# Performance work log

Hardware: AMD Instinct MI355X
Metric: run time of the kernel (lower is better)

The kernel has to match this reference:

```python
import jax, jax.numpy as jnp
import numpy as np

LN_EPS = 1e-12


def _layernorm(x, gamma, beta):
    mu = jnp.mean(x, axis=-1, keepdims=True)
    var = jnp.var(x, axis=-1, keepdims=True)
    return gamma * (x - mu) / jnp.sqrt(var + LN_EPS) + beta


def setup_inputs() -> dict:
    key = jax.random.key(0)
    ks = jax.random.split(key, 8)
    B, N, C, H = 8, 8192, 512, 8
    FFN = 4 * C
    s_attn = 1.0 / np.sqrt(C)
    s_ffn1 = 1.0 / np.sqrt(C)
    s_ffn2 = 1.0 / np.sqrt(FFN)
    return {
        "x": jax.random.normal(ks[0], (B, N, C), jnp.float32),
        "wq": jax.random.normal(ks[1], (C, C), jnp.float32) * s_attn,
        "bq": jnp.zeros((C,), jnp.float32),
        "wk": jax.random.normal(ks[2], (C, C), jnp.float32) * s_attn,
        "bk": jnp.zeros((C,), jnp.float32),
        "wv": jax.random.normal(ks[3], (C, C), jnp.float32) * s_attn,
        "bv": jnp.zeros((C,), jnp.float32),
        "wo": jax.random.normal(ks[4], (C, C), jnp.float32) * s_attn,
        "bo": jnp.zeros((C,), jnp.float32),
        "gamma1": jnp.ones((C,), jnp.float32),
        "beta1": jnp.zeros((C,), jnp.float32),
        "w_fc1": jax.random.normal(ks[5], (C, FFN), jnp.float32) * s_ffn1,
        "b_fc1": jnp.zeros((FFN,), jnp.float32),
        "w_fc2": jax.random.normal(ks[6], (FFN, C), jnp.float32) * s_ffn2,
        "b_fc2": jnp.zeros((C,), jnp.float32),
        "gamma2": jnp.ones((C,), jnp.float32),
        "beta2": jnp.zeros((C,), jnp.float32),
        "window_size": 64,
        "n_head": 8,
    }


def reference(x, wq, bq, wk, bk, wv, bv, wo, bo, gamma1, beta1,
              w_fc1, b_fc1, w_fc2, b_fc2, gamma2, beta2,
              window_size, n_head):
    B, N, C = x.shape
    ws = window_size
    H = n_head
    dh = C // H

    # window partition: [B, N, C] -> [B*N/ws, ws, C]
    xw = x.reshape(B * N // ws, ws, C)
    shortcut = xw

    # windowed multi-head self-attention
    q = (xw @ wq + bq).reshape(-1, ws, H, dh)
    k = (xw @ wk + bk).reshape(-1, ws, H, dh)
    v = (xw @ wv + bv).reshape(-1, ws, H, dh)
    scale = 1.0 / jnp.sqrt(jnp.asarray(dh, xw.dtype))
    attn = jnp.einsum('wqhd,wkhd->whqk', q, k) * scale  # [nw, H, ws, ws]
    attn = jax.nn.softmax(attn, axis=-1)
    out = jnp.einsum('whqk,wkhd->wqhd', attn, v).reshape(-1, ws, C)
    out = out @ wo + bo

    # residual + LN1
    h = _layernorm(out + shortcut, gamma1, beta1)

    # MLP (fc1 -> GELU -> fc2), residual + LN2
    ff = jax.nn.gelu(h @ w_fc1 + b_fc1, approximate=False) @ w_fc2 + b_fc2
    h = _layernorm(ff + h, gamma2, beta2)

    # window reverse: -> [B, N, C]
    return h.reshape(B, N, C)
```

## Files before the change

### kernel.cpp

```cpp
#include <hip/hip_runtime.h>

typedef __attribute__((ext_vector_type(8))) short bf16x8;
typedef __attribute__((ext_vector_type(4))) float f32x4;

__device__ __forceinline__ short f2b(float f) {
  unsigned u = __builtin_bit_cast(unsigned, f);
  unsigned r = (u + 0x7FFFu + ((u >> 16) & 1u)) >> 16;
  return (short)r;
}
__device__ __forceinline__ float b2f(short s) {
  unsigned u = ((unsigned)(unsigned short)s) << 16;
  return __builtin_bit_cast(float, u);
}

__device__ __forceinline__ void gload16(const void* g, void* l) {
  __builtin_amdgcn_global_load_lds(
      (const __attribute__((address_space(1))) void*)g,
      (__attribute__((address_space(3))) void*)l, 16, 0, 0);
}

__device__ __forceinline__ float gelu_f(float v) {
  float u = v * (0.7978845608f + 0.0356774081f * v * v);
  float a = fabsf(u);
  float e = __expf(-2.f * a);
  float t = (1.f - e) * __builtin_amdgcn_rcpf(1.f + e);
  t = (u < 0.f) ? -t : t;
  return 0.5f * v * (1.f + t);
}

__global__ void cvt_bf16_vec(const float* __restrict__ src, short* __restrict__ dst, long n) {
  long i = ((long)blockIdx.x * 256 + threadIdx.x) * 8;
  if (i >= n) return;
  f32x4 a = *(const f32x4*)(src + i);
  f32x4 b = *(const f32x4*)(src + i + 4);
  bf16x8 o;
#pragma unroll
  for (int j = 0; j < 4; j++) o[j] = f2b(a[j]);
#pragma unroll
  for (int j = 0; j < 4; j++) o[j + 4] = f2b(b[j]);
  *(bf16x8*)(dst + i) = o;
}

__global__ void transpose_cvt_t(const float* __restrict__ src, short* __restrict__ dst,
                                int K, int N) {
  __shared__ float tile[32][33];
  const int n0 = blockIdx.x * 32, k0 = blockIdx.y * 32;
  const int j = threadIdx.x & 31, i0 = threadIdx.x >> 5;
#pragma unroll
  for (int r = 0; r < 4; r++) {
    int i = i0 + r * 8;
    tile[i][j] = src[(long)(k0 + i) * N + n0 + j];
  }
  __syncthreads();
#pragma unroll
  for (int r = 0; r < 4; r++) {
    int i = i0 + r * 8;
    dst[(long)(n0 + i) * K + k0 + j] = f2b(tile[j][i]);
  }
}

__global__ void pack_bias3(const float* __restrict__ b0, const float* __restrict__ b1,
                           const float* __restrict__ b2, float* __restrict__ out) {
  int t = blockIdx.x * 256 + threadIdx.x;
  if (t >= 1536) return;
  out[t] = (t < 512) ? b0[t] : ((t < 1024) ? b1[t - 512] : b2[t - 1024]);
}

template <int EPI>
__global__ __launch_bounds__(256, 3) void gemm_bt(
    const short* __restrict__ A, const short* __restrict__ Bt,
    const float* __restrict__ bias, const float* __restrict__ resF,
    const short* __restrict__ resB, void* __restrict__ Cout, int K, int ldc, int gxN) {
  __shared__ short lds[3 * 8192];
  const int t = threadIdx.x;
  const int w = t >> 6, lane = t & 63;
  const int lr = lane & 15, lg = lane >> 4;

  const int nwg = gridDim.x;
  const int orig = blockIdx.x;
  const int q = nwg >> 3, r = nwg & 7, xcd = orig & 7, idx = orig >> 3;
  const int swz = (xcd < r ? xcd * (q + 1) : r * (q + 1) + (xcd - r) * q) + idx;
  const long m0 = (long)(swz / gxN) * 128;
  const int n0 = (swz % gxN) * 128;

  const int wm = (w >> 1) * 64, wn = (w & 1) * 64;

  f32x4 acc[4][4];
#pragma unroll
  for (int i = 0; i < 4; i++)
#pragma unroll
    for (int j = 0; j < 4; j++) acc[i][j] = f32x4{0.f, 0.f, 0.f, 0.f};

  const int srow = t >> 2;
  const int schunk = (t & 3) ^ ((t >> 3) & 3);
  const short* Ag = A + (m0 + srow) * (long)K + schunk * 8;
  const short* Bg = Bt + ((long)n0 + srow) * K + schunk * 8;
  const long half = (long)64 * K;

#define STAGE(b, kt)                                   \
  {                                                    \
    short* d = lds + (b) * 8192 + t * 8;               \
    gload16(Ag + (long)(kt) * 32, d);                  \
    gload16(Ag + half + (long)(kt) * 32, d + 2048);    \
    gload16(Bg + (long)(kt) * 32, d + 4096);           \
    gload16(Bg + half + (long)(kt) * 32, d + 6144);    \
  }

  const int xsw = (lg ^ ((lr >> 1) & 3)) * 8;
  const int aoff = (wm + lr) * 32 + xsw;
  const int boff = 4096 + (wn + lr) * 32 + xsw;

#define TILE_WAIT(WN)                                        \
  asm volatile("s_waitcnt vmcnt(" #WN ")" ::: "memory");     \
  __builtin_amdgcn_sched_barrier(0);                         \
  __builtin_amdgcn_s_barrier();                              \
  __builtin_amdgcn_sched_barrier(0);

#define BODY(CB)                                                               \
  {                                                                            \
    const short* Lb = lds + (CB) * 8192;                                       \
    bf16x8 a[4], b[4];                                                         \
    _Pragma("unroll") for (int mi = 0; mi < 4; mi++)                           \
        a[mi] = *(const bf16x8*)(Lb + aoff + mi * 512);                        \
    _Pragma("unroll") for (int nj = 0; nj < 4; nj++)                           \
        b[nj] = *(const bf16x8*)(Lb + boff + nj * 512);                        \
    __builtin_amdgcn_s_setprio(1);                                             \
    _Pragma("unroll") for (int mi = 0; mi < 4; mi++)                           \
        _Pragma("unroll") for (int nj = 0; nj < 4; nj++) acc[mi][nj] =         \
            __builtin_amdgcn_mfma_f32_16x16x32_bf16(a[mi], b[nj], acc[mi][nj], \
                                                    0, 0, 0);                  \
    __builtin_amdgcn_s_setprio(0);                                             \
  }

  const int NKT = K >> 5;
  STAGE(0, 0)
  STAGE(1, 1)

  int cb = 0, sb = 2;
  for (int kt = 0; kt < NKT - 1; ++kt) {
    TILE_WAIT(4)
    if (kt + 2 < NKT) STAGE(sb, kt + 2)
    BODY(cb)
    cb = (cb == 2) ? 0 : cb + 1;
    sb = (sb == 2) ? 0 : sb + 1;
  }
  TILE_WAIT(0)
  BODY(cb)
#undef STAGE
#undef TILE_WAIT
#undef BODY

  float bv[4];
#pragma unroll
  for (int nj = 0; nj < 4; nj++) bv[nj] = bias[n0 + wn + nj * 16 + lr];

#pragma unroll
  for (int mi = 0; mi < 4; mi++)
#pragma unroll
    for (int i = 0; i < 4; i++) {
      const long row = m0 + wm + mi * 16 + lg * 4 + i;
      const long rb = row * ldc + n0 + wn + lr;
      if (EPI == 0) {
        short* p = (short*)Cout + rb;
#pragma unroll
        for (int nj = 0; nj < 4; nj++) p[nj * 16] = f2b(acc[mi][nj][i] + bv[nj]);
      } else if (EPI == 1) {
        short* p = (short*)Cout + rb;
#pragma unroll
        for (int nj = 0; nj < 4; nj++) p[nj * 16] = f2b(gelu_f(acc[mi][nj][i] + bv[nj]));
      } else if (EPI == 2) {
        float* p = (float*)Cout + rb;
        const float* rp = resF + rb;
#pragma unroll
        for (int nj = 0; nj < 4; nj++) p[nj * 16] = acc[mi][nj][i] + bv[nj] + rp[nj * 16];
      } else {
        float* p = (float*)Cout + rb;
        const short* rp = resB + rb;
#pragma unroll
        for (int nj = 0; nj < 4; nj++)
          p[nj * 16] = acc[mi][nj][i] + bv[nj] + b2f(rp[nj * 16]);
      }
    }
}

__global__ __launch_bounds__(256, 2) void attn_win(const short* __restrict__ QKV,
                                                   short* __restrict__ AO) {
  __shared__ short Vs[64 * 72];
  __shared__ short Ps[64 * 72];
  const int t = threadIdx.x, w = t >> 6, lane = t & 63;
  const int lr = lane & 15, lg = lane >> 4;
  const long base = (long)blockIdx.x * 64 * 1536;
  const long obase = (long)blockIdx.x * 64 * 512;

  for (int h = 0; h < 8; h++) {
    const int co = h * 64;
#pragma unroll
    for (int it = 0; it < 2; it++) {
      int c = t + it * 256;
      int j = c >> 3, d0 = (c & 7) * 8;
      *(bf16x8*)(Vs + j * 72 + d0) =
          *(const bf16x8*)(QKV + base + (long)j * 1536 + 1024 + co + d0);
    }
    __syncthreads();

    bf16x8 qf[2], kf[4][2];
#pragma unroll
    for (int kb = 0; kb < 2; kb++)
      qf[kb] = *(const bf16x8*)(QKV + base + (long)(w * 16 + lr) * 1536 + co + kb * 32 + lg * 8);
#pragma unroll
    for (int nj = 0; nj < 4; nj++)
#pragma unroll
      for (int kb = 0; kb < 2; kb++)
        kf[nj][kb] = *(const bf16x8*)(QKV + base + (long)(nj * 16 + lr) * 1536 + 512 + co +
                                      kb * 32 + lg * 8);

    f32x4 s[4];
#pragma unroll
    for (int nj = 0; nj < 4; nj++) {
      s[nj] = f32x4{0.f, 0.f, 0.f, 0.f};
      s[nj] = __builtin_amdgcn_mfma_f32_16x16x32_bf16(qf[0], kf[nj][0], s[nj], 0, 0, 0);
      s[nj] = __builtin_amdgcn_mfma_f32_16x16x32_bf16(qf[1], kf[nj][1], s[nj], 0, 0, 0);
      s[nj] = s[nj] * 0.125f;
    }

#pragma unroll
    for (int i = 0; i < 4; i++) {
      float mx = fmaxf(fmaxf(s[0][i], s[1][i]), fmaxf(s[2][i], s[3][i]));
#pragma unroll
      for (int off = 1; off < 16; off <<= 1) mx = fmaxf(mx, __shfl_xor(mx, off, 64));
      float sum = 0.f;
#pragma unroll
      for (int nj = 0; nj < 4; nj++) {
        float p = __expf(s[nj][i] - mx);
        s[nj][i] = p;
        sum += p;
      }
#pragma unroll
      for (int off = 1; off < 16; off <<= 1) sum += __shfl_xor(sum, off, 64);
      float inv = 1.f / sum;
#pragma unroll
      for (int nj = 0; nj < 4; nj++) s[nj][i] *= inv;
    }

#pragma unroll
    for (int nj = 0; nj < 4; nj++)
#pragma unroll
      for (int i = 0; i < 4; i++)
        Ps[(w * 16 + lg * 4 + i) * 72 + nj * 16 + lr] = f2b(s[nj][i]);

    bf16x8 pa[2];
#pragma unroll
    for (int kb = 0; kb < 2; kb++)
      pa[kb] = *(const bf16x8*)(Ps + (w * 16 + lr) * 72 + kb * 32 + lg * 8);

    f32x4 o[4];
#pragma unroll
    for (int nb = 0; nb < 4; nb++) o[nb] = f32x4{0.f, 0.f, 0.f, 0.f};
#pragma unroll
    for (int kb = 0; kb < 2; kb++)
#pragma unroll
      for (int nb = 0; nb < 4; nb++) {
        bf16x8 vb;
#pragma unroll
        for (int jj = 0; jj < 8; jj++)
          vb[jj] = Vs[(kb * 32 + lg * 8 + jj) * 72 + nb * 16 + lr];
        o[nb] = __builtin_amdgcn_mfma_f32_16x16x32_bf16(pa[kb], vb, o[nb], 0, 0, 0);
      }

#pragma unroll
    for (int nb = 0; nb < 4; nb++)
#pragma unroll
      for (int i = 0; i < 4; i++)
        AO[obase + (long)(w * 16 + lg * 4 + i) * 512 + co + nb * 16 + lr] = f2b(o[nb][i]);
    __syncthreads();
  }
}

template <int OUTB>
__global__ __launch_bounds__(256, 4) void ln_rows(const float* __restrict__ Y,
                                                  const float* __restrict__ gamma,
                                                  const float* __restrict__ beta,
                                                  short* __restrict__ Hb,
                                                  float* __restrict__ Of) {
  const int w = threadIdx.x >> 6, lane = threadIdx.x & 63;
  const long row = (long)blockIdx.x * 4 + w;
  const float* y = Y + row * 512 + lane * 8;
  f32x4 a = *(const f32x4*)(y);
  f32x4 b = *(const f32x4*)(y + 4);
  float s = a[0] + a[1] + a[2] + a[3] + b[0] + b[1] + b[2] + b[3];
  float s2 = a[0] * a[0] + a[1] * a[1] + a[2] * a[2] + a[3] * a[3] + b[0] * b[0] +
             b[1] * b[1] + b[2] * b[2] + b[3] * b[3];
#pragma unroll
  for (int off = 1; off < 64; off <<= 1) {
    s += __shfl_xor(s, off, 64);
    s2 += __shfl_xor(s2, off, 64);
  }
  float mu = s * (1.f / 512.f);
  float var = s2 * (1.f / 512.f) - mu * mu;
  float rstd = rsqrtf(fmaxf(var, 0.f) + 1e-12f);
  const int c0 = lane * 8;
  f32x4 ga = *(const f32x4*)(gamma + c0), gb = *(const f32x4*)(gamma + c0 + 4);
  f32x4 ba = *(const f32x4*)(beta + c0), bb = *(const f32x4*)(beta + c0 + 4);
  if (OUTB) {
    bf16x8 o;
#pragma unroll
    for (int j = 0; j < 4; j++) o[j] = f2b(ga[j] * ((a[j] - mu) * rstd) + ba[j]);
#pragma unroll
    for (int j = 0; j < 4; j++) o[j + 4] = f2b(gb[j] * ((b[j] - mu) * rstd) + bb[j]);
    *(bf16x8*)(Hb + row * 512 + c0) = o;
  } else {
    f32x4 o0, o1;
#pragma unroll
    for (int j = 0; j < 4; j++) o0[j] = ga[j] * ((a[j] - mu) * rstd) + ba[j];
#pragma unroll
    for (int j = 0; j < 4; j++) o1[j] = gb[j] * ((b[j] - mu) * rstd) + bb[j];
    *(f32x4*)(Of + row * 512 + c0) = o0;
    *(f32x4*)(Of + row * 512 + c0 + 4) = o1;
  }
}

extern "C" void kernel_launch(void* const* d_in, const int* in_sizes, int n_in,
                              void* d_out, int out_size, void* d_ws, size_t ws_size,
                              hipStream_t stream) {
  (void)in_sizes; (void)n_in; (void)out_size;
  const float* x = (const float*)d_in[0];
  const float* wq = (const float*)d_in[1];
  const float* bq = (const float*)d_in[2];
  const float* wk = (const float*)d_in[3];
  const float* bk = (const float*)d_in[4];
  const float* wv = (const float*)d_in[5];
  const float* bv = (const float*)d_in[6];
  const float* wo = (const float*)d_in[7];
  const float* bo = (const float*)d_in[8];
  const float* g1 = (const float*)d_in[9];
  const float* be1 = (const float*)d_in[10];
  const float* wfc1 = (const float*)d_in[11];
  const float* bfc1 = (const float*)d_in[12];
  const float* wfc2 = (const float*)d_in[13];
  const float* bfc2 = (const float*)d_in[14];
  const float* g2 = (const float*)d_in[15];
  const float* be2 = (const float*)d_in[16];

  const long T = 65536;
  char* ws = (char*)d_ws;

  short* WQKVT = (short*)(ws);
  short* WOT = WQKVT + 1536 * 512;
  short* WFC1T = WOT + 512 * 512;
  short* WFC2T = WFC1T + 2048 * 512;
  float* BQKV = (float*)(WFC2T + 512 * 2048);
  size_t woff = ((size_t)((char*)(BQKV + 1536) - ws) + 255) & ~(size_t)255;

  size_t avail = (ws_size > woff) ? (ws_size - woff) : 0;
  long Tc = T;
  while (Tc > 128 && (size_t)Tc * 7168 > avail) Tc >>= 1;
  const long nch = T / Tc;

  char* R0 = ws + woff;
  char* R1 = R0 + (size_t)Tc * 4096;
  char* R2 = R1 + (size_t)Tc * 2048;

  short* QKV = (short*)R0;
  float* Y1 = (float*)R0;
  short* FF1 = (short*)R0;
  short* XB = (short*)R1;
  short* AO = (short*)R1;
  float* Y2 = (float*)R1;
  short* H = (short*)R2;

  transpose_cvt_t<<<dim3(16, 16), 256, 0, stream>>>(wq, WQKVT, 512, 512);
  transpose_cvt_t<<<dim3(16, 16), 256, 0, stream>>>(wk, WQKVT + 512 * 512, 512, 512);
  transpose_cvt_t<<<dim3(16, 16), 256, 0, stream>>>(wv, WQKVT + 1024 * 512, 512, 512);
  transpose_cvt_t<<<dim3(16, 16), 256, 0, stream>>>(wo, WOT, 512, 512);
  transpose_cvt_t<<<dim3(64, 16), 256, 0, stream>>>(wfc1, WFC1T, 512, 2048);
  transpose_cvt_t<<<dim3(16, 64), 256, 0, stream>>>(wfc2, WFC2T, 2048, 512);
  pack_bias3<<<6, 256, 0, stream>>>(bq, bk, bv, BQKV);

  for (long c = 0; c < nch; c++) {
    const long t0 = c * Tc;
    const int mb = (int)(Tc / 128);
    cvt_bf16_vec<<<(int)(Tc / 4), 256, 0, stream>>>(x + t0 * 512, XB, Tc * 512);
    gemm_bt<0><<<mb * 12, 256, 0, stream>>>(XB, WQKVT, BQKV, nullptr, nullptr,
                                            (void*)QKV, 512, 1536, 12);
    attn_win<<<(int)(Tc / 64), 256, 0, stream>>>(QKV, AO);
    gemm_bt<2><<<mb * 4, 256, 0, stream>>>(AO, WOT, bo, x + t0 * 512, nullptr,
                                           (void*)Y1, 512, 512, 4);
    ln_rows<1><<<(int)(Tc / 4), 256, 0, stream>>>(Y1, g1, be1, H, nullptr);
    gemm_bt<1><<<mb * 16, 256, 0, stream>>>(H, WFC1T, bfc1, nullptr, nullptr,
                                            (void*)FF1, 512, 2048, 16);
    gemm_bt<3><<<mb * 4, 256, 0, stream>>>(FF1, WFC2T, bfc2, nullptr, H, (void*)Y2,
                                           2048, 512, 4);
    ln_rows<0><<<(int)(Tc / 4), 256, 0, stream>>>(Y2, g2, be2, nullptr,
                                                  (float*)d_out + t0 * 512);
  }
}
```

Before: 819.6 us.

## Load GEMM B operand directly into registers and stage only A through LDS

The GEMM mainloop stops staging the B tile through shared memory. Each wave now loads its B fragments straight from global memory into registers, one k-step ahead, using even/odd register buffers. Only A still goes through a 3-slot LDS ring, read with inline ds_read_b128 and explicit vmcnt/lgkmcnt waits. This halves LDS use and removes the B LDS round-trip. The cost is uncoalesced, redundant per-wave global loads of B, more VGPR pressure, and fragile hand-counted waitcnt logic that assumes an even number of k-tiles.

```diff
diff --git a/kernel.cpp b/kernel.cpp
--- a/kernel.cpp
+++ b/kernel.cpp
@@ -71,7 +71,7 @@
     const short* __restrict__ A, const short* __restrict__ Bt,
     const float* __restrict__ bias, const float* __restrict__ resF,
     const short* __restrict__ resB, void* __restrict__ Cout, int K, int ldc, int gxN) {
-  __shared__ short lds[3 * 8192];
+  __shared__ short lds[3 * 4096];
   const int t = threadIdx.x;
   const int w = t >> 6, lane = t & 63;
   const int lr = lane & 15, lg = lane >> 4;
@@ -94,61 +94,72 @@
   const int srow = t >> 2;
   const int schunk = (t & 3) ^ ((t >> 3) & 3);
   const short* Ag = A + (m0 + srow) * (long)K + schunk * 8;
-  const short* Bg = Bt + ((long)n0 + srow) * K + schunk * 8;
   const long half = (long)64 * K;
 
-#define STAGE(b, kt)                                   \
-  {                                                    \
-    short* d = lds + (b) * 8192 + t * 8;               \
-    gload16(Ag + (long)(kt) * 32, d);                  \
-    gload16(Ag + half + (long)(kt) * 32, d + 2048);    \
-    gload16(Bg + (long)(kt) * 32, d + 4096);           \
-    gload16(Bg + half + (long)(kt) * 32, d + 6144);    \
-  }
-
-  const int xsw = (lg ^ ((lr >> 1) & 3)) * 8;
-  const int aoff = (wm + lr) * 32 + xsw;
-  const int boff = 4096 + (wn + lr) * 32 + xsw;
-
-#define TILE_WAIT(WN)                                        \
-  asm volatile("s_waitcnt vmcnt(" #WN ")" ::: "memory");     \
-  __builtin_amdgcn_sched_barrier(0);                         \
-  __builtin_amdgcn_s_barrier();                              \
-  __builtin_amdgcn_sched_barrier(0);
-
-#define BODY(CB)                                                               \
-  {                                                                            \
-    const short* Lb = lds + (CB) * 8192;                                       \
-    bf16x8 a[4], b[4];                                                         \
-    _Pragma("unroll") for (int mi = 0; mi < 4; mi++)                           \
-        a[mi] = *(const bf16x8*)(Lb + aoff + mi * 512);                        \
-    _Pragma("unroll") for (int nj = 0; nj < 4; nj++)                           \
-        b[nj] = *(const bf16x8*)(Lb + boff + nj * 512);                        \
-    __builtin_amdgcn_s_setprio(1);                                             \
-    _Pragma("unroll") for (int mi = 0; mi < 4; mi++)                           \
-        _Pragma("unroll") for (int nj = 0; nj < 4; nj++) acc[mi][nj] =         \
-            __builtin_amdgcn_mfma_f32_16x16x32_bf16(a[mi], b[nj], acc[mi][nj], \
-                                                    0, 0, 0);                  \
-    __builtin_amdgcn_s_setprio(0);                                             \
-  }
+#define STAGE(slot, kt)                                 \
+  {                                                     \
+    short* d = lds + (slot) * 4096 + t * 8;             \
+    gload16(Ag + (long)(kt) * 32, d);                   \
+    gload16(Ag + half + (long)(kt) * 32, d + 2048);     \
+  }
+
+  const short* Bg = Bt + ((long)n0 + wn + lr) * K + lg * 8;
+#define LOADB(B, kt)                                                        \
+  {                                                                         \
+    _Pragma("unroll") for (int nj = 0; nj < 4; nj++) B[nj] =                \
+        *(const bf16x8*)(Bg + (long)nj * 16 * K + (long)(kt) * 32);         \
+  }
+
+  const unsigned abase =
+      (unsigned)(uintptr_t)lds + ((wm + lr) * 32 + (lg ^ ((lr >> 1) & 3)) * 8) * 2;
 
   const int NKT = K >> 5;
   STAGE(0, 0)
   STAGE(1, 1)
-
-  int cb = 0, sb = 2;
-  for (int kt = 0; kt < NKT - 1; ++kt) {
-    TILE_WAIT(4)
-    if (kt + 2 < NKT) STAGE(sb, kt + 2)
-    BODY(cb)
-    cb = (cb == 2) ? 0 : cb + 1;
-    sb = (sb == 2) ? 0 : sb + 1;
-  }
-  TILE_WAIT(0)
-  BODY(cb)
+  bf16x8 bE[4], bO[4];
+  LOADB(bE, 0)
+  __builtin_amdgcn_sched_barrier(0);
+
+#define BODY(TT, BC, BN)                                                      \
+  {                                                                           \
+    const int tb = ((TT) + 1 < NKT) ? (TT) + 1 : NKT - 1;                     \
+    const int ts = ((TT) + 2 < NKT) ? (TT) + 2 : NKT - 1;                     \
+    LOADB(BN, tb)                                                             \
+    __builtin_amdgcn_sched_barrier(0);                                        \
+    asm volatile("s_waitcnt vmcnt(10)");                                      \
+    __builtin_amdgcn_s_barrier();                                             \
+    __builtin_amdgcn_sched_barrier(0);                                        \
+    STAGE(((TT) + 2) % 3, ts)                                                 \
+    __builtin_amdgcn_sched_barrier(0);                                        \
+    const unsigned ab = abase + ((TT) % 3) * 8192;                            \
+    bf16x8 a0, a1, a2, a3;                                                    \
+    asm volatile("ds_read_b128 %0, %1" : "=v"(a0) : "v"(ab));                 \
+    asm volatile("ds_read_b128 %0, %1 offset:1024" : "=v"(a1) : "v"(ab));     \
+    asm volatile("ds_read_b128 %0, %1 offset:2048" : "=v"(a2) : "v"(ab));     \
+    asm volatile("ds_read_b128 %0, %1 offset:3072" : "=v"(a3) : "v"(ab));     \
+    asm volatile("s_waitcnt lgkmcnt(0)");                                     \
+    __builtin_amdgcn_sched_barrier(0);                                        \
+    __builtin_amdgcn_s_setprio(1);                                            \
+    _Pragma("unroll") for (int nj = 0; nj < 4; nj++) {                        \
+      acc[0][nj] =                                                            \
+          __builtin_amdgcn_mfma_f32_16x16x32_bf16(a0, BC[nj], acc[0][nj], 0, 0, 0); \
+      acc[1][nj] =                                                            \
+          __builtin_amdgcn_mfma_f32_16x16x32_bf16(a1, BC[nj], acc[1][nj], 0, 0, 0); \
+      acc[2][nj] =                                                            \
+          __builtin_amdgcn_mfma_f32_16x16x32_bf16(a2, BC[nj], acc[2][nj], 0, 0, 0); \
+      acc[3][nj] =                                                            \
+          __builtin_amdgcn_mfma_f32_16x16x32_bf16(a3, BC[nj], acc[3][nj], 0, 0, 0); \
+    }                                                                         \
+    __builtin_amdgcn_s_setprio(0);                                            \
+  }
+
+  for (int tt = 0; tt < NKT; tt += 2) {
+    BODY(tt, bE, bO)
+    BODY(tt + 1, bO, bE)
+  }
+#undef BODY
 #undef STAGE
-#undef TILE_WAIT
-#undef BODY
+#undef LOADB
 
   float bv[4];
 #pragma unroll
```

Measured after the change: 1.171 ms. 1.43x slower.
